# Kernel tuning notes

Hardware: AMD Instinct MI355X
Metric: run time of the kernel (lower is better)

Reference implementation:

```python
import jax, jax.numpy as jnp
import numpy as np

DIM, DEPTH, MULT = 512, 3, 4
E = 2 ** DEPTH            # 8 experts
HID = MULT * DIM          # 2048
B, S = 4, 1024


def setup_inputs() -> dict:
    key = jax.random.key(0)
    ks = jax.random.split(key, 7)
    sd = 1.0 / np.sqrt(DIM)
    sh = 1.0 / np.sqrt(HID)
    return {
        "x": jax.random.normal(ks[0], (B, S, DIM), dtype=jnp.float32),
        "rw": jax.random.normal(ks[1], (E - 1, DIM), dtype=jnp.float32) * sd,
        "rb": jax.random.normal(ks[2], (E - 1,), dtype=jnp.float32) * sd,
        "w1": jax.random.normal(ks[3], (E, DIM, HID), dtype=jnp.float32) * sd,
        "b1": jax.random.normal(ks[4], (E, HID), dtype=jnp.float32) * sd,
        "w2": jax.random.normal(ks[5], (E, HID, DIM), dtype=jnp.float32) * sh,
        "b2": jax.random.normal(ks[6], (E, DIM), dtype=jnp.float32) * sh,
    }


def _leaf_probs(flat_x, rw, rb):
    # Binary-tree soft routing: level d has 2**d routers at offset 2**d - 1.
    n_tok = flat_x.shape[0]
    leaf = jnp.ones((n_tok, 1), dtype=flat_x.dtype)
    for d in range(DEPTH):
        off, n = 2 ** d - 1, 2 ** d
        logits = flat_x @ rw[off:off + n].T + rb[off:off + n]   # [N, n]
        p = jax.nn.sigmoid(logits)
        # child probs: left = 1-p, right = p
        leaf = (leaf[:, :, None] * jnp.stack([1.0 - p, p], axis=2)).reshape(n_tok, 2 * n)
    return leaf  # [N, E]


def reference(x, rw, rb, w1, b1, w2, b2):
    b, s, dim = x.shape
    flat_x = x.reshape(b * s, dim)                               # [N, D]
    leaf_probs = _leaf_probs(flat_x, rw, rb)                     # [N, E]
    # Dense evaluation of all experts (soft-routing training path).
    h = jnp.einsum('nd,edh->neh', flat_x, w1) + b1[None]         # [N, E, H]
    h = jax.nn.gelu(h, approximate=False)                        # torch nn.GELU (erf)
    y = jnp.einsum('neh,ehd->ned', h, w2) + b2[None]             # [N, E, D]
    out = jnp.einsum('ned,ne->nd', y, leaf_probs)                # [N, D]
    return out.reshape(b, s, dim)
```

## Files before the change

kernel.cpp:

```cpp
#include <hip/hip_runtime.h>
#include <hip/hip_bf16.h>
#include <hip/hip_fp16.h>

#define DIM 512
#define HID 2048
#define NE 8
#define NTOK 4096

typedef _Float16 v8h __attribute__((ext_vector_type(8)));
typedef float v4f __attribute__((ext_vector_type(4)));

__device__ __forceinline__ void load16(const void* g, void* l) {
  __builtin_amdgcn_global_load_lds(
      (const __attribute__((address_space(1))) unsigned int*)g,
      (__attribute__((address_space(3))) unsigned int*)l, 16, 0, 0);
}

__device__ __forceinline__ float gelu_erf(float v) {
  float z = v * 0.70710678118654752f;
  float az = __builtin_fabsf(z);
  float t = __builtin_amdgcn_rcpf(1.0f + 0.3275911f * az);
  float poly = 1.061405429f;
  poly = poly * t - 1.453152027f;
  poly = poly * t + 1.421413741f;
  poly = poly * t - 0.284496736f;
  poly = poly * t + 0.254829592f;
  poly = poly * t;
  float erf_abs = 1.0f - poly * __expf(-z * z);
  float erf = __builtin_copysignf(erf_abs, z);
  return 0.5f * v * (1.0f + erf);
}

__global__ __launch_bounds__(256) void routing_kernel(const float* __restrict__ x,
                                                      const float* __restrict__ rw,
                                                      const float* __restrict__ rb,
                                                      float* __restrict__ leaf,
                                                      _Float16* __restrict__ xh) {
  const int lane = threadIdx.x & 63;
  const int wave = threadIdx.x >> 6;
  const int n = (blockIdx.x << 2) + wave;
  const float4* xv = (const float4*)(x + (size_t)n * DIM);
  const float4 x0 = xv[lane * 2], x1 = xv[lane * 2 + 1];
  v8h o;
  o[0] = (_Float16)x0.x; o[1] = (_Float16)x0.y; o[2] = (_Float16)x0.z; o[3] = (_Float16)x0.w;
  o[4] = (_Float16)x1.x; o[5] = (_Float16)x1.y; o[6] = (_Float16)x1.z; o[7] = (_Float16)x1.w;
  *(v8h*)(xh + (size_t)n * DIM + lane * 8) = o;
  float logits[7];
#pragma unroll
  for (int rr = 0; rr < 7; ++rr) {
    const float4* wv = (const float4*)(rw + rr * DIM);
    const float4 w0 = wv[lane * 2], w1v = wv[lane * 2 + 1];
    float s = x0.x * w0.x + x0.y * w0.y + x0.z * w0.z + x0.w * w0.w +
              x1.x * w1v.x + x1.y * w1v.y + x1.z * w1v.z + x1.w * w1v.w;
#pragma unroll
    for (int o2 = 32; o2; o2 >>= 1) s += __shfl_xor(s, o2, 64);
    logits[rr] = s + rb[rr];
  }
  if (lane < NE) {
    const int eidx = lane;
    const float p0 = 1.f / (1.f + __expf(-logits[0]));
    float f = ((eidx >> 2) & 1) ? p0 : 1.f - p0;
    const float p1 = 1.f / (1.f + __expf(-logits[1 + (eidx >> 2)]));
    f *= ((eidx >> 1) & 1) ? p1 : 1.f - p1;
    const float p2 = 1.f / (1.f + __expf(-logits[3 + (eidx >> 1)]));
    f *= (eidx & 1) ? p2 : 1.f - p2;
    leaf[(size_t)n * NE + eidx] = f;
  }
}

__global__ __launch_bounds__(256) void transpose_cvt2_kernel(const float* __restrict__ w1,
                                                             _Float16* __restrict__ w1t,
                                                             const float* __restrict__ w2,
                                                             _Float16* __restrict__ w2t) {
  int bx = blockIdx.x;
  const float* in;
  _Float16* outp;
  int R, C;
  if (bx < 4096) { in = w1; outp = w1t; R = DIM; C = HID; }
  else { bx -= 4096; in = w2; outp = w2t; R = HID; C = DIM; }
  const int e = bx >> 9;
  const int rem = bx & 511;
  const int tiles_r = R >> 6;
  const int rt = rem % tiles_r;
  const int ct = rem / tiles_r;
  const int r0 = rt << 6, c0 = ct << 5;
  const size_t ebase = (size_t)e * R * C;

  __shared__ float tile[32][65];
  const int tid = threadIdx.x;
#pragma unroll
  for (int it = 0; it < 2; ++it) {
    const int s = tid + (it << 8);
    const int row = s >> 3, cq = s & 7;
    const float4 v = *(const float4*)(in + ebase + (size_t)(r0 + row) * C + c0 + (cq << 2));
    tile[(cq << 2) + 0][row] = v.x;
    tile[(cq << 2) + 1][row] = v.y;
    tile[(cq << 2) + 2][row] = v.z;
    tile[(cq << 2) + 3][row] = v.w;
  }
  __syncthreads();
  const int c = tid >> 3, seg = tid & 7;
  v8h h;
#pragma unroll
  for (int u = 0; u < 8; ++u) h[u] = (_Float16)tile[c][(seg << 3) + u];
  *(v8h*)(outp + ebase + (size_t)(c0 + c) * R + r0 + (seg << 3)) = h;
}

__global__ __launch_bounds__(256) void out_init_kernel(const float* __restrict__ leaf,
                                                       const float* __restrict__ b2,
                                                       float* __restrict__ out) {
  const int g = blockIdx.x * 256 + threadIdx.x;
  const int n = g >> 7, dq = g & 127;
  const float* lp = leaf + (size_t)n * NE;
  float4 acc = {0.f, 0.f, 0.f, 0.f};
#pragma unroll
  for (int e = 0; e < NE; ++e) {
    const float pe = lp[e];
    const float4 bv = *(const float4*)(b2 + (size_t)e * DIM + (dq << 2));
    acc.x += pe * bv.x; acc.y += pe * bv.y; acc.z += pe * bv.z; acc.w += pe * bv.w;
  }
  *(float4*)(out + (size_t)n * DIM + (dq << 2)) = acc;
}

__global__ __launch_bounds__(256) void gemm1_kernel(const _Float16* __restrict__ xh,
                                                    const _Float16* __restrict__ w1t,
                                                    const float* __restrict__ b1,
                                                    const float* __restrict__ leaf,
                                                    _Float16* __restrict__ H) {
  const int bx = blockIdx.x;
  const int e = bx & 7;
  const int t = bx >> 3;
  const int mt = t & 31;
  const int nt = t >> 5;
  const int m0 = mt << 7, n0 = nt << 7;

  __shared__ alignas(16) _Float16 As[128 * 64];
  __shared__ alignas(16) _Float16 Bs[128 * 64];

  const int tid = threadIdx.x;
  const int lane = tid & 63;
  const int wave = tid >> 6;
  const int qm = wave >> 1, qn = wave & 1;
  const int r = lane & 15, q = lane >> 4;

  const _Float16* Ab = xh + (size_t)m0 * DIM;
  const _Float16* Bb = w1t + ((size_t)e * HID + n0) * DIM;

  v4f acc[4][4];
#pragma unroll
  for (int i = 0; i < 4; ++i)
#pragma unroll
    for (int j = 0; j < 4; ++j) acc[i][j] = v4f{0.f, 0.f, 0.f, 0.f};

  const int ch0 = wave << 8;
  for (int k0 = 0; k0 < DIM; k0 += 64) {
#pragma unroll
    for (int i = 0; i < 4; ++i) {
      const int ch = ch0 + (i << 6) + lane;
      const int row = ch >> 3;
      const int c8 = (ch & 7) ^ (row & 7);
      load16(Ab + (size_t)row * DIM + k0 + (c8 << 3), As + (size_t)ch * 8);
      load16(Bb + (size_t)row * DIM + k0 + (c8 << 3), Bs + (size_t)ch * 8);
    }
    __syncthreads();
#pragma unroll
    for (int ks = 0; ks < 64; ks += 32) {
      v8h a[4], b[4];
#pragma unroll
      for (int i = 0; i < 4; ++i) {
        const int row = (qm << 6) + (i << 4) + r;
        const int s = (((ks >> 3) + q) ^ (row & 7));
        a[i] = *(const v8h*)(As + (row << 6) + (s << 3));
      }
#pragma unroll
      for (int j = 0; j < 4; ++j) {
        const int row = (qn << 6) + (j << 4) + r;
        const int s = (((ks >> 3) + q) ^ (row & 7));
        b[j] = *(const v8h*)(Bs + (row << 6) + (s << 3));
      }
#pragma unroll
      for (int i = 0; i < 4; ++i)
#pragma unroll
        for (int j = 0; j < 4; ++j)
          acc[i][j] = __builtin_amdgcn_mfma_f32_16x16x32_f16(a[i], b[j], acc[i][j], 0, 0, 0);
    }
    __syncthreads();
  }

  const float* b1e = b1 + (size_t)e * HID;
  _Float16* He = H + (size_t)e * NTOK * HID;
  float bias[4];
#pragma unroll
  for (int j = 0; j < 4; ++j) bias[j] = b1e[n0 + (qn << 6) + (j << 4) + r];
#pragma unroll
  for (int i = 0; i < 4; ++i) {
    const int rowb = m0 + (qm << 6) + (i << 4) + (q << 2);
#pragma unroll
    for (int rr = 0; rr < 4; ++rr) {
      const int row = rowb + rr;
      const float p = leaf[(size_t)row * NE + e];
#pragma unroll
      for (int j = 0; j < 4; ++j) {
        const int col = n0 + (qn << 6) + (j << 4) + r;
        He[(size_t)row * HID + col] = (_Float16)(p * gelu_erf(acc[i][j][rr] + bias[j]));
      }
    }
  }
}

__global__ __launch_bounds__(256) void gemm2_kernel(const _Float16* __restrict__ H,
                                                    const _Float16* __restrict__ w2t,
                                                    float* __restrict__ out) {
  const int bx = blockIdx.x;
  const int mt = bx & 31;
  const int dt = (bx >> 5) & 3;
  const int sp = bx >> 7;
  const int m0 = mt << 7, d0 = dt << 7;
  const int kbase = sp << 12;

  __shared__ alignas(16) _Float16 As[128 * 64];
  __shared__ alignas(16) _Float16 Bs[128 * 64];

  const int tid = threadIdx.x;
  const int lane = tid & 63;
  const int wave = tid >> 6;
  const int qm = wave >> 1, qn = wave & 1;
  const int r = lane & 15, q = lane >> 4;

  v4f acc[4][4];
#pragma unroll
  for (int i = 0; i < 4; ++i)
#pragma unroll
    for (int j = 0; j < 4; ++j) acc[i][j] = v4f{0.f, 0.f, 0.f, 0.f};

  const int ch0 = wave << 8;
  for (int kk = 0; kk < 4096; kk += 64) {
    const int kg = kbase + kk;
    const int e = kg >> 11;
    const int kl = kg & 2047;
    const _Float16* Ab = H + ((size_t)e * NTOK + m0) * HID + kl;
    const _Float16* Bb = w2t + ((size_t)e * DIM + d0) * HID + kl;
#pragma unroll
    for (int i = 0; i < 4; ++i) {
      const int ch = ch0 + (i << 6) + lane;
      const int row = ch >> 3;
      const int c8 = (ch & 7) ^ (row & 7);
      load16(Ab + (size_t)row * HID + (c8 << 3), As + (size_t)ch * 8);
      load16(Bb + (size_t)row * HID + (c8 << 3), Bs + (size_t)ch * 8);
    }
    __syncthreads();
#pragma unroll
    for (int ks = 0; ks < 64; ks += 32) {
      v8h a[4], b[4];
#pragma unroll
      for (int i = 0; i < 4; ++i) {
        const int row = (qm << 6) + (i << 4) + r;
        const int s = (((ks >> 3) + q) ^ (row & 7));
        a[i] = *(const v8h*)(As + (row << 6) + (s << 3));
      }
#pragma unroll
      for (int j = 0; j < 4; ++j) {
        const int row = (qn << 6) + (j << 4) + r;
        const int s = (((ks >> 3) + q) ^ (row & 7));
        b[j] = *(const v8h*)(Bs + (row << 6) + (s << 3));
      }
#pragma unroll
      for (int i = 0; i < 4; ++i)
#pragma unroll
        for (int j = 0; j < 4; ++j)
          acc[i][j] = __builtin_amdgcn_mfma_f32_16x16x32_f16(a[i], b[j], acc[i][j], 0, 0, 0);
    }
    __syncthreads();
  }

#pragma unroll
  for (int i = 0; i < 4; ++i) {
    const int rowb = m0 + (qm << 6) + (i << 4) + (q << 2);
#pragma unroll
    for (int j = 0; j < 4; ++j) {
      const int col = d0 + (qn << 6) + (j << 4) + r;
#pragma unroll
      for (int rr = 0; rr < 4; ++rr)
        atomicAdd(out + (size_t)(rowb + rr) * DIM + col, acc[i][j][rr]);
    }
  }
}

extern "C" void kernel_launch(void* const* d_in, const int* in_sizes, int n_in,
                              void* d_out, int out_size, void* d_ws, size_t ws_size,
                              hipStream_t stream) {
  const float* x  = (const float*)d_in[0];
  const float* rw = (const float*)d_in[1];
  const float* rb = (const float*)d_in[2];
  const float* w1 = (const float*)d_in[3];
  const float* b1 = (const float*)d_in[4];
  const float* w2 = (const float*)d_in[5];
  const float* b2 = (const float*)d_in[6];
  float* out = (float*)d_out;

  char* ws = (char*)d_ws;
  const size_t xh_bytes   = (size_t)NTOK * DIM * 2;
  const size_t w1t_bytes  = (size_t)NE * HID * DIM * 2;
  const size_t w2t_bytes  = (size_t)NE * DIM * HID * 2;
  const size_t leaf_bytes = (size_t)NTOK * NE * 4;
  const size_t H_bytes    = (size_t)NE * NTOK * HID * 2;
  _Float16* xh   = (_Float16*)(ws);
  _Float16* w1t  = (_Float16*)(ws + xh_bytes);
  _Float16* w2t  = (_Float16*)(ws + xh_bytes + w1t_bytes);
  float*    leaf = (float*)(ws + xh_bytes + w1t_bytes + w2t_bytes);
  _Float16* Hbuf = (_Float16*)(ws + xh_bytes + w1t_bytes + w2t_bytes + leaf_bytes);
  if (ws_size < xh_bytes + w1t_bytes + w2t_bytes + leaf_bytes + H_bytes) return;

  routing_kernel<<<1024, 256, 0, stream>>>(x, rw, rb, leaf, xh);
  transpose_cvt2_kernel<<<8192, 256, 0, stream>>>(w1, w1t, w2, w2t);
  out_init_kernel<<<2048, 256, 0, stream>>>(leaf, b2, out);
  gemm1_kernel<<<4096, 256, 0, stream>>>(xh, w1t, b1, leaf, Hbuf);
  gemm2_kernel<<<512, 256, 0, stream>>>(Hbuf, w2t, out);
}
```

Before: 340.0 us.

## Use tanh-form GELU, precompute load addresses, and split gemm2 per expert

Replaces the erf-polynomial GELU with the tanh approximation written as v*sigmoid(u), which cuts the epilogue transcendental and polynomial work. Both GEMMs precompute global and LDS fragment pointers so the unrolled K loop does less integer address arithmetic. gemm2 now splits K per expert (1024 blocks, each covering one expert's 2048-wide K) rather than two-expert chunks, which doubles parallelism and doubles atomic traffic into the output. The tanh GELU departs from the exact erf form the reference uses, so it adds a small numerical error.

```diff
diff --git a/kernel.cpp b/kernel.cpp
--- a/kernel.cpp
+++ b/kernel.cpp
@@ -16,19 +16,11 @@
       (__attribute__((address_space(3))) unsigned int*)l, 16, 0, 0);
 }
 
-__device__ __forceinline__ float gelu_erf(float v) {
-  float z = v * 0.70710678118654752f;
-  float az = __builtin_fabsf(z);
-  float t = __builtin_amdgcn_rcpf(1.0f + 0.3275911f * az);
-  float poly = 1.061405429f;
-  poly = poly * t - 1.453152027f;
-  poly = poly * t + 1.421413741f;
-  poly = poly * t - 0.284496736f;
-  poly = poly * t + 0.254829592f;
-  poly = poly * t;
-  float erf_abs = 1.0f - poly * __expf(-z * z);
-  float erf = __builtin_copysignf(erf_abs, z);
-  return 0.5f * v * (1.0f + erf);
+__device__ __forceinline__ float gelu_fast(float v) {
+  float v2 = v * v;
+  float u = v * __builtin_fmaf(0.07135481627f, v2, 1.5957691216f);
+  float t = __expf(-u);
+  return v * __builtin_amdgcn_rcpf(1.0f + t);
 }
 
 __global__ __launch_bounds__(256) void routing_kernel(const float* __restrict__ x,
@@ -143,8 +135,32 @@
   const int qm = wave >> 1, qn = wave & 1;
   const int r = lane & 15, q = lane >> 4;
 
-  const _Float16* Ab = xh + (size_t)m0 * DIM;
-  const _Float16* Bb = w1t + ((size_t)e * HID + n0) * DIM;
+  const _Float16* pa[4];
+  const _Float16* pb[4];
+  _Float16* la[4];
+  _Float16* lb[4];
+#pragma unroll
+  for (int i = 0; i < 4; ++i) {
+    const int ch = (wave << 8) + (i << 6) + lane;
+    const int row = ch >> 3;
+    const int c8 = (ch & 7) ^ (row & 7);
+    pa[i] = xh + (size_t)(m0 + row) * DIM + (c8 << 3);
+    pb[i] = w1t + ((size_t)e * HID + n0 + row) * DIM + (c8 << 3);
+    la[i] = As + (size_t)ch * 8;
+    lb[i] = Bs + (size_t)ch * 8;
+  }
+  const _Float16* fa[2][4];
+  const _Float16* fb[2][4];
+#pragma unroll
+  for (int ks = 0; ks < 2; ++ks) {
+#pragma unroll
+    for (int i = 0; i < 4; ++i) {
+      const int rowa = (qm << 6) + (i << 4) + r;
+      fa[ks][i] = As + (rowa << 6) + ((((ks << 2) + q) ^ (rowa & 7)) << 3);
+      const int rowb = (qn << 6) + (i << 4) + r;
+      fb[ks][i] = Bs + (rowb << 6) + ((((ks << 2) + q) ^ (rowb & 7)) << 3);
+    }
+  }
 
   v4f acc[4][4];
 #pragma unroll
@@ -152,32 +168,21 @@
 #pragma unroll
     for (int j = 0; j < 4; ++j) acc[i][j] = v4f{0.f, 0.f, 0.f, 0.f};
 
-  const int ch0 = wave << 8;
-  for (int k0 = 0; k0 < DIM; k0 += 64) {
+#pragma unroll
+  for (int kk = 0; kk < 8; ++kk) {
 #pragma unroll
     for (int i = 0; i < 4; ++i) {
-      const int ch = ch0 + (i << 6) + lane;
-      const int row = ch >> 3;
-      const int c8 = (ch & 7) ^ (row & 7);
-      load16(Ab + (size_t)row * DIM + k0 + (c8 << 3), As + (size_t)ch * 8);
-      load16(Bb + (size_t)row * DIM + k0 + (c8 << 3), Bs + (size_t)ch * 8);
+      load16(pa[i] + kk * 64, la[i]);
+      load16(pb[i] + kk * 64, lb[i]);
     }
     __syncthreads();
 #pragma unroll
-    for (int ks = 0; ks < 64; ks += 32) {
+    for (int ks = 0; ks < 2; ++ks) {
       v8h a[4], b[4];
 #pragma unroll
-      for (int i = 0; i < 4; ++i) {
-        const int row = (qm << 6) + (i << 4) + r;
-        const int s = (((ks >> 3) + q) ^ (row & 7));
-        a[i] = *(const v8h*)(As + (row << 6) + (s << 3));
-      }
-#pragma unroll
-      for (int j = 0; j < 4; ++j) {
-        const int row = (qn << 6) + (j << 4) + r;
-        const int s = (((ks >> 3) + q) ^ (row & 7));
-        b[j] = *(const v8h*)(Bs + (row << 6) + (s << 3));
-      }
+      for (int i = 0; i < 4; ++i) a[i] = *(const v8h*)fa[ks][i];
+#pragma unroll
+      for (int j = 0; j < 4; ++j) b[j] = *(const v8h*)fb[ks][j];
 #pragma unroll
       for (int i = 0; i < 4; ++i)
 #pragma unroll
@@ -199,11 +204,10 @@
     for (int rr = 0; rr < 4; ++rr) {
       const int row = rowb + rr;
       const float p = leaf[(size_t)row * NE + e];
-#pragma unroll
-      for (int j = 0; j < 4; ++j) {
-        const int col = n0 + (qn << 6) + (j << 4) + r;
-        He[(size_t)row * HID + col] = (_Float16)(p * gelu_erf(acc[i][j][rr] + bias[j]));
-      }
+      _Float16* hp = He + (size_t)row * HID + n0 + (qn << 6) + r;
+#pragma unroll
+      for (int j = 0; j < 4; ++j)
+        hp[j << 4] = (_Float16)(p * gelu_fast(acc[i][j][rr] + bias[j]));
     }
   }
 }
@@ -212,11 +216,10 @@
                                                     const _Float16* __restrict__ w2t,
                                                     float* __restrict__ out) {
   const int bx = blockIdx.x;
-  const int mt = bx & 31;
-  const int dt = (bx >> 5) & 3;
-  const int sp = bx >> 7;
+  const int e = bx & 7;
+  const int mt = (bx >> 3) & 31;
+  const int dt = bx >> 8;
   const int m0 = mt << 7, d0 = dt << 7;
-  const int kbase = sp << 12;
 
   __shared__ alignas(16) _Float16 As[128 * 64];
   __shared__ alignas(16) _Float16 Bs[128 * 64];
@@ -227,50 +230,65 @@
   const int qm = wave >> 1, qn = wave & 1;
   const int r = lane & 15, q = lane >> 4;
 
+  const _Float16* pa[4];
+  const _Float16* pb[4];
+  _Float16* la[4];
+  _Float16* lb[4];
+#pragma unroll
+  for (int i = 0; i < 4; ++i) {
+    const int ch = (wave << 8) + (i << 6) + lane;
+    const int row = ch >> 3;
+    const int c8 = (ch & 7) ^ (row & 7);
+    pa[i] = H + ((size_t)e * NTOK + m0 + row) * HID + (c8 << 3);
+    pb[i] = w2t + ((size_t)e * DIM + d0 + row) * HID + (c8 << 3);
+    la[i] = As + (size_t)ch * 8;
+    lb[i] = Bs + (size_t)ch * 8;
+  }
+  const _Float16* fa[2][4];
+  const _Float16* fb[2][4];
+#pragma unroll
+  for (int ks = 0; ks < 2; ++ks) {
+#pragma unroll
+    for (int i = 0; i < 4; ++i) {
+      const int rowa = (qm << 6) + (i << 4) + r;
+      fa[ks][i] = As + (rowa << 6) + ((((ks << 2) + q) ^ (rowa & 7)) << 3);
+      const int rowb = (qn << 6) + (i << 4) + r;
+      fb[ks][i] = Bs + (rowb << 6) + ((((ks << 2) + q) ^ (rowb & 7)) << 3);
+    }
+  }
+
   v4f acc[4][4];
 #pragma unroll
   for (int i = 0; i < 4; ++i)
 #pragma unroll
     for (int j = 0; j < 4; ++j) acc[i][j] = v4f{0.f, 0.f, 0.f, 0.f};
 
-  const int ch0 = wave << 8;
-  for (int kk = 0; kk < 4096; kk += 64) {
-    const int kg = kbase + kk;
-    const int e = kg >> 11;
-    const int kl = kg & 2047;
-    const _Float16* Ab = H + ((size_t)e * NTOK + m0) * HID + kl;
-    const _Float16* Bb = w2t + ((size_t)e * DIM + d0) * HID + kl;
-#pragma unroll
-    for (int i = 0; i < 4; ++i) {
-      const int ch = ch0 + (i << 6) + lane;
-      const int row = ch >> 3;
-      const int c8 = (ch & 7) ^ (row & 7);
-      load16(Ab + (size_t)row * HID + (c8 << 3), As + (size_t)ch * 8);
-      load16(Bb + (size_t)row * HID + (c8 << 3), Bs + (size_t)ch * 8);
-    }
-    __syncthreads();
-#pragma unroll
-    for (int ks = 0; ks < 64; ks += 32) {
-      v8h a[4], b[4];
+  for (int ko = 0; ko < 4; ++ko) {
+#pragma unroll
+    for (int u = 0; u < 8; ++u) {
 #pragma unroll
       for (int i = 0; i < 4; ++i) {
-        const int row = (qm << 6) + (i << 4) + r;
-        const int s = (((ks >> 3) + q) ^ (row & 7));
-        a[i] = *(const v8h*)(As + (row << 6) + (s << 3));
+        load16(pa[i] + u * 64, la[i]);
+        load16(pb[i] + u * 64, lb[i]);
       }
-#pragma unroll
-      for (int j = 0; j < 4; ++j) {
-        const int row = (qn << 6) + (j << 4) + r;
-        const int s = (((ks >> 3) + q) ^ (row & 7));
-        b[j] = *(const v8h*)(Bs + (row << 6) + (s << 3));
+      __syncthreads();
+#pragma unroll
+      for (int ks = 0; ks < 2; ++ks) {
+        v8h a[4], b[4];
+#pragma unroll
+        for (int i = 0; i < 4; ++i) a[i] = *(const v8h*)fa[ks][i];
+#pragma unroll
+        for (int j = 0; j < 4; ++j) b[j] = *(const v8h*)fb[ks][j];
+#pragma unroll
+        for (int i = 0; i < 4; ++i)
+#pragma unroll
+          for (int j = 0; j < 4; ++j)
+            acc[i][j] = __builtin_amdgcn_mfma_f32_16x16x32_f16(a[i], b[j], acc[i][j], 0, 0, 0);
       }
-#pragma unroll
-      for (int i = 0; i < 4; ++i)
-#pragma unroll
-        for (int j = 0; j < 4; ++j)
-          acc[i][j] = __builtin_amdgcn_mfma_f32_16x16x32_f16(a[i], b[j], acc[i][j], 0, 0, 0);
-    }
-    __syncthreads();
+      __syncthreads();
+    }
+#pragma unroll
+    for (int i = 0; i < 4; ++i) { pa[i] += 512; pb[i] += 512; }
   }
 
 #pragma unroll
@@ -315,5 +333,5 @@
   transpose_cvt2_kernel<<<8192, 256, 0, stream>>>(w1, w1t, w2, w2t);
   out_init_kernel<<<2048, 256, 0, stream>>>(leaf, b2, out);
   gemm1_kernel<<<4096, 256, 0, stream>>>(xh, w1t, b1, leaf, Hbuf);
-  gemm2_kernel<<<512, 256, 0, stream>>>(Hbuf, w2t, out);
-}
+  gemm2_kernel<<<1024, 256, 0, stream>>>(Hbuf, w2t, out);
+}
```

Result: no change. 341.8 us (+0.5%).
